# Optimization experiments

Hardware: AMD Instinct MI355X
Metric: run time of the kernel (lower is better)

## Reference

```python
import jax, jax.numpy as jnp
import numpy as np

B, S, HID = 8, 4096, 1024
NH, HD = 16, 64  # heads, head_dim
LN_EPS = 1e-12


def setup_inputs() -> dict:
    key = jax.random.key(0)
    ks = jax.random.split(key, 12)
    sd = 1.0 / np.sqrt(HID)
    return {
        "input_tensor": jax.random.normal(ks[0], (B, S, HID), jnp.float32),
        "attention_mask": jnp.ones((B, S), jnp.int32),
        "ln_gamma": jnp.ones((HID,), jnp.float32),
        "ln_beta": jnp.zeros((HID,), jnp.float32),
        "Wq": jax.random.normal(ks[1], (HID, HID), jnp.float32) * sd,
        "bq": jnp.zeros((HID,), jnp.float32),
        "Wk": jax.random.normal(ks[2], (HID, HID), jnp.float32) * sd,
        "bk": jnp.zeros((HID,), jnp.float32),
        "Wv": jax.random.normal(ks[3], (HID, HID), jnp.float32) * sd,
        "bv": jnp.zeros((HID,), jnp.float32),
        "Wo": jax.random.normal(ks[4], (HID, HID), jnp.float32) * sd,
        "bo": jnp.zeros((HID,), jnp.float32),
    }


def _layernorm(x, g, b):
    mu = jnp.mean(x, axis=-1, keepdims=True)
    var = jnp.mean(jnp.square(x - mu), axis=-1, keepdims=True)
    return (x - mu) * jax.lax.rsqrt(var + LN_EPS) * g + b


def reference(input_tensor, attention_mask, ln_gamma, ln_beta,
              Wq, bq, Wk, bk, Wv, bv, Wo, bo):
    # NOTE: attention_mask is accepted but unused, matching the original module.
    x = input_tensor
    x_norm = _layernorm(x, ln_gamma, ln_beta)
    # projections: query from normalized input, key/value from raw input
    q = (x_norm @ Wq.T + bq).reshape(B, S, NH, HD).transpose(0, 2, 1, 3)  # bhsd
    k = (x @ Wk.T + bk).reshape(B, S, NH, HD).transpose(0, 2, 1, 3)      # bhsd
    v = (x @ Wv.T + bv).reshape(B, S, NH, HD).transpose(0, 2, 1, 3)      # bhsd

    eq = jax.nn.elu(q)
    ek = jax.nn.elu(k)
    # per-token L2 norms over head_dim (matches norm over d in both layouts)
    eq = eq / jnp.linalg.norm(eq, axis=-1, keepdims=True)
    ek = ek / jnp.linalg.norm(ek, axis=-1, keepdims=True)

    # linear attention: Q (K^T V), never materializing [S,S]
    kv = jnp.einsum('bhsd,bhse->bhde', ek, v)          # [B,H,d,d]
    ctx = jnp.einsum('bhsd,bhde->bhse', eq, kv) / np.sqrt(HD)

    ctx = ctx.transpose(0, 2, 1, 3).reshape(B, S, HID)
    out = ctx @ Wo.T + bo
    return out + x  # residual (dropouts are identity in eval mode)
```

## Files before the change

### kernel.cpp

```cpp
#include <hip/hip_runtime.h>

typedef unsigned short u16;
typedef unsigned int   u32;
typedef __attribute__((ext_vector_type(8))) __bf16 bf16x8;
typedef __attribute__((ext_vector_type(4))) float  f32x4;

#define BQ   8
#define SQ   4096
#define NHQ  16
#define HIDD 1024
#define TOKN 32768

__device__ __forceinline__ u16 f2bf(float f){
  u32 u = __builtin_bit_cast(u32, f);
  u += 0x7fffu + ((u >> 16) & 1u);
  return (u16)(u >> 16);
}
__device__ __forceinline__ float bf2f(u16 h){
  return __builtin_bit_cast(float, (u32)h << 16);
}
__device__ __forceinline__ void gl16(const void* g, void* l){
  __builtin_amdgcn_global_load_lds((const __attribute__((address_space(1))) void*)g,
                                   (__attribute__((address_space(3))) void*)l, 16, 0, 0);
}
#define MFMA(a,b,c) __builtin_amdgcn_mfma_f32_16x16x32_bf16((a),(b),(c),0,0,0)

__global__ __launch_bounds__(256) void k_cast3(const float* __restrict__ wk,
    const float* __restrict__ wv, const float* __restrict__ wo,
    u16* __restrict__ okv, u16* __restrict__ oo){
  const int sel = blockIdx.x >> 10;
  const int i = ((blockIdx.x & 1023) << 8) + threadIdx.x;
  const float* in = (sel == 0) ? wk : (sel == 1) ? wv : wo;
  u16* o = (sel == 0) ? okv : (sel == 1) ? (okv + 1024 * 1024) : oo;
  float4 v = ((const float4*)in)[i];
  ushort4 r;
  r.x = f2bf(v.x); r.y = f2bf(v.y); r.z = f2bf(v.z); r.w = f2bf(v.w);
  ((ushort4*)o)[i] = r;
}

__global__ __launch_bounds__(256) void k_wq(const float* __restrict__ Wq,
    const float* __restrict__ gam, const float* __restrict__ bet, const float* __restrict__ bq,
    u16* __restrict__ wqb, float* __restrict__ cq, float* __restrict__ dq){
  const int j = blockIdx.x, t = threadIdx.x;
  const float4 wv = ((const float4*)(Wq + (size_t)j * 1024))[t];
  const float4 gv = ((const float4*)gam)[t];
  const float4 bv = ((const float4*)bet)[t];
  ushort4 r;
  r.x = f2bf(wv.x * gv.x); r.y = f2bf(wv.y * gv.y);
  r.z = f2bf(wv.z * gv.z); r.w = f2bf(wv.w * gv.w);
  ((ushort4*)(wqb + (size_t)j * 1024))[t] = r;
  float sc = bf2f(r.x) + bf2f(r.y) + bf2f(r.z) + bf2f(r.w);
  float sd = wv.x * bv.x + wv.y * bv.y + wv.z * bv.z + wv.w * bv.w;
  #pragma unroll
  for (int o = 1; o < 64; o <<= 1){ sc += __shfl_xor(sc, o); sd += __shfl_xor(sd, o); }
  __shared__ float sm[8];
  const int lane = t & 63, wid = t >> 6;
  if (lane == 0){ sm[wid] = sc; sm[wid + 4] = sd; }
  __syncthreads();
  if (t == 0){
    cq[j] = sm[0] + sm[1] + sm[2] + sm[3];
    dq[j] = sm[4] + sm[5] + sm[6] + sm[7] + bq[j];
  }
}

__global__ __launch_bounds__(256) void k_ln(const float* __restrict__ x,
    u16* __restrict__ xbf, float* __restrict__ mur, float* __restrict__ rsd){
  const int row = blockIdx.x, t = threadIdx.x;
  const float4 v = ((const float4*)(x + (size_t)row * HIDD))[t];
  float s  = v.x + v.y + v.z + v.w;
  float ss = v.x*v.x + v.y*v.y + v.z*v.z + v.w*v.w;
  #pragma unroll
  for (int o = 1; o < 64; o <<= 1){ s += __shfl_xor(s, o); ss += __shfl_xor(ss, o); }
  __shared__ float sm[8];
  const int lane = t & 63, wid = t >> 6;
  if (lane == 0){ sm[wid] = s; sm[wid + 4] = ss; }
  __syncthreads();
  s  = sm[0] + sm[1] + sm[2] + sm[3];
  ss = sm[4] + sm[5] + sm[6] + sm[7];
  const float mu   = s * (1.f / 1024.f);
  const float var  = ss * (1.f / 1024.f) - mu * mu;
  const float rstd = rsqrtf(var + 1e-12f);
  if (t == 0){ mur[row] = mu * rstd; rsd[row] = rstd; }
  ushort4 xo;
  xo.x = f2bf(v.x); xo.y = f2bf(v.y); xo.z = f2bf(v.z); xo.w = f2bf(v.w);
  ((ushort4*)(xbf + (size_t)row * HIDD))[t] = xo;
}

struct GP {
  const u16* A; const u16* W; const float* b1; const float* b2;
  int nsplit, lgNB, LDC, nblk; u16* outb; u16* voutT;
  const float* cq; const float* dq; const float* mur; const float* rsd;
};

template<int RES, int SPLIT>
__global__ __launch_bounds__(512, 2) void k_gemm256(GP p0, GP p1, int seg0,
    const u16* __restrict__ residb, float* __restrict__ outf){
  __shared__ union {
    u16 st[2][2][16384];
    float cep[8][1056];
    float cep2[8][2112];
  } sm;

  const GP& p = (blockIdx.x < seg0) ? p0 : p1;
  const int bseg = (blockIdx.x < seg0) ? blockIdx.x : blockIdx.x - seg0;
  const u16* __restrict__ A = p.A;
  const u16* __restrict__ W = p.W;
  const int lgNB = p.lgNB, LDC = p.LDC;

  const int wg = ((bseg & 7) * (p.nblk >> 3)) + (bseg >> 3);
  const int m0 = (wg >> lgNB) << 8;
  const int n0 = (wg & ((1 << lgNB) - 1)) << 8;

  const int t = threadIdx.x, lane = t & 63, wid = t >> 6;
  const int ln15 = lane & 15, hi = lane >> 4;
  const int wr = wid >> 2, wc = wid & 3;
  const int lg = lane & 7, lr = lane >> 3;

  auto stage = [&](int buf, int op, const u16* __restrict__ src, int rowoff, int kt){
    #pragma unroll
    for (int i = 0; i < 4; i++){
      const int cb  = ((i << 3) + wid) << 6;
      const int row = (cb >> 3) + lr;
      const int g   = lg ^ lr;
      gl16(src + (size_t)(rowoff + row) * HIDD + (kt << 6) + (g << 3),
           &sm.st[buf][op][cb << 3]);
    }
  };
  auto stageH = [&](int buf, int op, const u16* __restrict__ src, int rowoff, int kt, int half){
    #pragma unroll
    for (int i2 = 0; i2 < 2; i2++){
      const int i = (half << 1) + i2;
      const int cb  = ((i << 3) + wid) << 6;
      const int row = (cb >> 3) + lr;
      const int g   = lg ^ lr;
      gl16(src + (size_t)(rowoff + row) * HIDD + (kt << 6) + (g << 3),
           &sm.st[buf][op][cb << 3]);
    }
  };
  #define RD_A(c,m,ks) (*(const bf16x8*)&sm.st[c][0][(((wr << 7) + ((m) << 4) + ln15) << 6) + \
      (((((ks) << 2) + hi) ^ (lane & 7)) << 3)])
  #define RD_B(c,n,ks) (*(const bf16x8*)&sm.st[c][1][(((wc << 6) + ((n) << 4) + ln15) << 6) + \
      (((((ks) << 2) + hi) ^ (lane & 7)) << 3)])
  #define BARF do { asm volatile("" ::: "memory"); __builtin_amdgcn_s_barrier(); asm volatile("" ::: "memory"); } while(0)

  f32x4 acc[8][4] = {};

  stage(0, 0, A, m0, 0);
  stage(0, 1, W, n0, 0);
  stage(1, 1, W, n0, 1);
  asm volatile("s_waitcnt vmcnt(4)" ::: "memory");
  BARF;

  const int NT = HIDD / 64;
  if constexpr (SPLIT == 0){
    for (int kt = 0; kt < NT; ++kt){
      const int c = kt & 1;
      bf16x8 af[4][2], bq[4][2];
      #pragma unroll
      for (int m = 0; m < 4; m++){ af[m][0] = RD_A(c, m, 0); af[m][1] = RD_A(c, m, 1); }
      #pragma unroll
      for (int n = 0; n < 4; n++){ bq[n][0] = RD_B(c, n, 0); bq[n][1] = RD_B(c, n, 1); }
      const int ka = kt + 1 < NT ? kt + 1 : NT - 1;
      stage(c ^ 1, 0, A, m0, ka);
      __builtin_amdgcn_s_setprio(1);
      #pragma unroll
      for (int m = 0; m < 4; m++)
        #pragma unroll
        for (int n = 0; n < 4; n++){
          acc[m][n] = MFMA(af[m][0], bq[n][0], acc[m][n]);
          acc[m][n] = MFMA(af[m][1], bq[n][1], acc[m][n]);
        }
      __builtin_amdgcn_s_setprio(0);
      BARF;
      #pragma unroll
      for (int m = 0; m < 4; m++){ af[m][0] = RD_A(c, m + 4, 0); af[m][1] = RD_A(c, m + 4, 1); }
      const int kb = kt + 2 < NT ? kt + 2 : NT - 1;
      stage(c, 1, W, n0, kb);
      __builtin_amdgcn_s_setprio(1);
      #pragma unroll
      for (int m = 0; m < 4; m++)
        #pragma unroll
        for (int n = 0; n < 4; n++){
          acc[m + 4][n] = MFMA(af[m][0], bq[n][0], acc[m + 4][n]);
          acc[m + 4][n] = MFMA(af[m][1], bq[n][1], acc[m + 4][n]);
        }
      __builtin_amdgcn_s_setprio(0);
      asm volatile("s_waitcnt vmcnt(4)" ::: "memory");
      BARF;
    }
  } else {
    for (int kt = 0; kt < NT; ++kt){
      const int c = kt & 1;
      const int ka  = kt + 1 < NT ? kt + 1 : NT - 1;
      const int kb2 = kt + 2 < NT ? kt + 2 : NT - 1;
      bf16x8 af[2][2], bq[4][2];
      af[0][0] = RD_A(c, 0, 0); af[0][1] = RD_A(c, 0, 1);
      af[1][0] = RD_A(c, 1, 0); af[1][1] = RD_A(c, 1, 1);
      #pragma unroll
      for (int n = 0; n < 4; n++){ bq[n][0] = RD_B(c, n, 0); bq[n][1] = RD_B(c, n, 1); }
      stageH(c ^ 1, 0, A, m0, ka, 0);
      __builtin_amdgcn_s_setprio(1);
      #pragma unroll
      for (int m = 0; m < 2; m++)
        #pragma unroll
        for (int n = 0; n < 4; n++){
          acc[m][n] = MFMA(af[m][0], bq[n][0], acc[m][n]);
          acc[m][n] = MFMA(af[m][1], bq[n][1], acc[m][n]);
        }
      __builtin_amdgcn_s_setprio(0);
      BARF;
      af[0][0] = RD_A(c, 2, 0); af[0][1] = RD_A(c, 2, 1);
      af[1][0] = RD_A(c, 3, 0); af[1][1] = RD_A(c, 3, 1);
      stageH(c ^ 1, 0, A, m0, ka, 1);
      __builtin_amdgcn_s_setprio(1);
      #pragma unroll
      for (int m = 0; m < 2; m++)
        #pragma unroll
        for (int n = 0; n < 4; n++){
          acc[m + 2][n] = MFMA(af[m][0], bq[n][0], acc[m + 2][n]);
          acc[m + 2][n] = MFMA(af[m][1], bq[n][1], acc[m + 2][n]);
        }
      __builtin_amdgcn_s_setprio(0);
      BARF;
      af[0][0] = RD_A(c, 4, 0); af[0][1] = RD_A(c, 4, 1);
      af[1][0] = RD_A(c, 5, 0); af[1][1] = RD_A(c, 5, 1);
      stageH(c, 1, W, n0, kb2, 0);
      __builtin_amdgcn_s_setprio(1);
      #pragma unroll
      for (int m = 0; m < 2; m++)
        #pragma unroll
        for (int n = 0; n < 4; n++){
          acc[m + 4][n] = MFMA(af[m][0], bq[n][0], acc[m + 4][n]);
          acc[m + 4][n] = MFMA(af[m][1], bq[n][1], acc[m + 4][n]);
        }
      __builtin_amdgcn_s_setprio(0);
      BARF;
      af[0][0] = RD_A(c, 6, 0); af[0][1] = RD_A(c, 6, 1);
      af[1][0] = RD_A(c, 7, 0); af[1][1] = RD_A(c, 7, 1);
      stageH(c, 1, W, n0, kb2, 1);
      __builtin_amdgcn_s_setprio(1);
      #pragma unroll
      for (int m = 0; m < 2; m++)
        #pragma unroll
        for (int n = 0; n < 4; n++){
          acc[m + 6][n] = MFMA(af[m][0], bq[n][0], acc[m + 6][n]);
          acc[m + 6][n] = MFMA(af[m][1], bq[n][1], acc[m + 6][n]);
        }
      __builtin_amdgcn_s_setprio(0);
      asm volatile("s_waitcnt vmcnt(4)" ::: "memory");
      BARF;
    }
  }
  #undef RD_A
  #undef RD_B

  asm volatile("s_waitcnt vmcnt(0)" ::: "memory");
  BARF;

  const float* bp = (n0 < p.nsplit) ? p.b1 : (p.b2 - p.nsplit);
  float bn[4];
  #pragma unroll
  for (int n = 0; n < 4; n++) bn[n] = bp[n0 + (wc << 6) + (n << 4) + ln15];

  if constexpr (RES){
    float* cw = &sm.cep[wid][0];
    const int rr = lane >> 3, cb8 = (lane & 7) << 3;
    #pragma unroll
    for (int m = 0; m < 8; m++){
      #pragma unroll
      for (int n = 0; n < 4; n++)
        #pragma unroll
        for (int r = 0; r < 4; r++)
          cw[((hi << 2) + r) * 66 + (n << 4) + ln15] = acc[m][n][r] + bn[n];
      #pragma unroll
      for (int j = 0; j < 2; j++){
        const int row = (j << 3) + rr;
        const size_t gr = (size_t)(m0 + (wr << 7) + (m << 4) + row);
        const size_t gidx = gr * LDC + n0 + (wc << 6) + cb8;
        const size_t ridx = gr * HIDD + n0 + (wc << 6) + cb8;
        const uint4 rv = *(const uint4*)&residb[ridx];
        const u32 rr4[4] = {rv.x, rv.y, rv.z, rv.w};
        float4 o0, o1;
        o0.x = cw[row * 66 + cb8 + 0] + bf2f((u16)(rr4[0] & 0xffff));
        o0.y = cw[row * 66 + cb8 + 1] + bf2f((u16)(rr4[0] >> 16));
        o0.z = cw[row * 66 + cb8 + 2] + bf2f((u16)(rr4[1] & 0xffff));
        o0.w = cw[row * 66 + cb8 + 3] + bf2f((u16)(rr4[1] >> 16));
        o1.x = cw[row * 66 + cb8 + 4] + bf2f((u16)(rr4[2] & 0xffff));
        o1.y = cw[row * 66 + cb8 + 5] + bf2f((u16)(rr4[2] >> 16));
        o1.z = cw[row * 66 + cb8 + 6] + bf2f((u16)(rr4[3] & 0xffff));
        o1.w = cw[row * 66 + cb8 + 7] + bf2f((u16)(rr4[3] >> 16));
        *(float4*)&outf[gidx]     = o0;
        *(float4*)&outf[gidx + 4] = o1;
      }
    }
  } else if (p.voutT != nullptr && n0 >= p.nsplit){
    float* cw = &sm.cep2[wid][0];
    const int e0 = n0 - p.nsplit + (wc << 6);
    const int hh = e0 >> 6;
    u16* vt = p.voutT;
    #pragma unroll
    for (int mp = 0; mp < 4; mp++){
      #pragma unroll
      for (int mh = 0; mh < 2; mh++){
        const int m = (mp << 1) + mh;
        #pragma unroll
        for (int n = 0; n < 4; n++)
          #pragma unroll
          for (int r = 0; r < 4; r++)
            cw[((mh << 4) + (hi << 2) + r) * 66 + (n << 4) + ln15] = acc[m][n][r] + bn[n];
      }
      const int rg0 = m0 + (wr << 7) + (mp << 5);
      const int bb = rg0 >> 12, s0 = rg0 & 4095;
      u16* dst = vt + (((size_t)(bb << 4) + hh) * 64 + lane) * SQ + s0;
      #pragma unroll
      for (int j = 0; j < 4; j++){
        u32 ro[4];
        #pragma unroll
        for (int q = 0; q < 4; q++){
          float v0 = cw[((j << 3) + 2 * q    ) * 66 + lane];
          float v1 = cw[((j << 3) + 2 * q + 1) * 66 + lane];
          ro[q] = (u32)f2bf(v0) | ((u32)f2bf(v1) << 16);
        }
        uint4 o; o.x = ro[0]; o.y = ro[1]; o.z = ro[2]; o.w = ro[3];
        *(uint4*)&dst[j << 3] = o;
      }
    }
  } else {
    float* cw = &sm.cep[wid][0];
    const int rr = lane >> 3, cb8 = (lane & 7) << 3;
    u16* outb = p.outb;
    if (p.cq != nullptr){
      float cqn[4], dqn[4];
      #pragma unroll
      for (int n = 0; n < 4; n++){
        const int col = n0 + (wc << 6) + (n << 4) + ln15;
        cqn[n] = p.cq[col]; dqn[n] = p.dq[col];
      }
      #pragma unroll
      for (int m = 0; m < 8; m++){
        #pragma unroll
        for (int r = 0; r < 4; r++){
          const int grow = m0 + (wr << 7) + (m << 4) + (hi << 2) + r;
          const float mu = p.mur[grow], rs = p.rsd[grow];
          #pragma unroll
          for (int n = 0; n < 4; n++)
            cw[((hi << 2) + r) * 66 + (n << 4) + ln15] = rs * acc[m][n][r] - mu * cqn[n] + dqn[n];
        }
        #pragma unroll
        for (int j = 0; j < 2; j++){
          const int row = (j << 3) + rr;
          u32 ro[4];
          #pragma unroll
          for (int pq = 0; pq < 4; pq++){
            float v0 = cw[row * 66 + cb8 + 2 * pq];
            float v1 = cw[row * 66 + cb8 + 2 * pq + 1];
            ro[pq] = (u32)f2bf(v0) | ((u32)f2bf(v1) << 16);
          }
          uint4 o; o.x = ro[0]; o.y = ro[1]; o.z = ro[2]; o.w = ro[3];
          *(uint4*)&outb[(size_t)(m0 + (wr << 7) + (m << 4) + row) * LDC
                         + n0 + (wc << 6) + cb8] = o;
        }
      }
    } else {
      #pragma unroll
      for (int m = 0; m < 8; m++){
        #pragma unroll
        for (int n = 0; n < 4; n++)
          #pragma unroll
          for (int r = 0; r < 4; r++)
            cw[((hi << 2) + r) * 66 + (n << 4) + ln15] = acc[m][n][r] + bn[n];
        #pragma unroll
        for (int j = 0; j < 2; j++){
          const int row = (j << 3) + rr;
          u32 ro[4];
          #pragma unroll
          for (int pq = 0; pq < 4; pq++){
            float v0 = cw[row * 66 + cb8 + 2 * pq];
            float v1 = cw[row * 66 + cb8 + 2 * pq + 1];
            ro[pq] = (u32)f2bf(v0) | ((u32)f2bf(v1) << 16);
          }
          uint4 o; o.x = ro[0]; o.y = ro[1]; o.z = ro[2]; o.w = ro[3];
          *(uint4*)&outb[(size_t)(m0 + (wr << 7) + (m << 4) + row) * LDC
                         + n0 + (wc << 6) + cb8] = o;
        }
      }
    }
  }
  #undef BARF
}

__global__ __launch_bounds__(256) void k_transposeK(const u16* __restrict__ kb,
                                                    u16* __restrict__ ekT){
  __shared__ float tile[64][65];
  __shared__ float pr[64][4];
  __shared__ float rn[64];
  const int sb = blockIdx.x << 6, h = blockIdx.y, b = blockIdx.z;
  const int t = threadIdx.x;
  {
    const int tok = t >> 2, q = t & 3;
    const u16* src = kb + (size_t)(b * SQ + sb + tok) * 1024 + (h << 6) + (q << 4);
    uint4 u0 = *(const uint4*)src;
    uint4 u1 = *(const uint4*)(src + 8);
    u32 uu[8] = {u0.x, u0.y, u0.z, u0.w, u1.x, u1.y, u1.z, u1.w};
    float ss = 0.f;
    #pragma unroll
    for (int i = 0; i < 8; i++){
      float f0 = bf2f((u16)(uu[i] & 0xffff));
      float f1 = bf2f((u16)(uu[i] >> 16));
      f0 = f0 > 0.f ? f0 : expm1f(f0);
      f1 = f1 > 0.f ? f1 : expm1f(f1);
      ss += f0 * f0 + f1 * f1;
      tile[tok][(q << 4) + 2*i]     = f0;
      tile[tok][(q << 4) + 2*i + 1] = f1;
    }
    pr[tok][q] = ss;
  }
  __syncthreads();
  if (t < 64) rn[t] = rsqrtf(pr[t][0] + pr[t][1] + pr[t][2] + pr[t][3]);
  __syncthreads();
  const int d = t >> 2, sq2 = (t & 3) << 4;
  u16* dst = ekT + ((size_t)(b * NHQ + h) * 64 + d) * SQ + sb + sq2;
  u32 ro[8];
  #pragma unroll
  for (int i = 0; i < 8; i++){
    float v0 = tile[sq2 + 2*i][d]     * rn[sq2 + 2*i];
    float v1 = tile[sq2 + 2*i + 1][d] * rn[sq2 + 2*i + 1];
    ro[i] = (u32)f2bf(v0) | ((u32)f2bf(v1) << 16);
  }
  uint4 o0; o0.x = ro[0]; o0.y = ro[1]; o0.z = ro[2]; o0.w = ro[3];
  uint4 o1; o1.x = ro[4]; o1.y = ro[5]; o1.z = ro[6]; o1.w = ro[7];
  *(uint4*)dst = o0;
  *(uint4*)(dst + 8) = o1;
}

__global__ __launch_bounds__(256) void k_kv(const u16* __restrict__ vT, const u16* __restrict__ ekT,
                                            u16* __restrict__ kvT){
  const int bh = blockIdx.x;
  const u16* Av = vT  + (size_t)bh * 64 * SQ;
  const u16* Bk = ekT + (size_t)bh * 64 * SQ;
  const int lane = threadIdx.x & 63, wid = threadIdx.x >> 6;
  const int ln15 = lane & 15, hi = lane >> 4;
  f32x4 acc[4][4] = {};
  const int kb = wid << 10;
  for (int ks = 0; ks < 32; ++ks){
    const int k0 = kb + (ks << 5) + (hi << 3);
    bf16x8 af[4], bfr[4];
    #pragma unroll
    for (int m = 0; m < 4; m++) af[m]  = *(const bf16x8*)(Av + (size_t)((m << 4) + ln15) * SQ + k0);
    #pragma unroll
    for (int n = 0; n < 4; n++) bfr[n] = *(const bf16x8*)(Bk + (size_t)((n << 4) + ln15) * SQ + k0);
    #pragma unroll
    for (int m = 0; m < 4; m++)
      #pragma unroll
      for (int n = 0; n < 4; n++)
        acc[m][n] = MFMA(af[m], bfr[n], acc[m][n]);
  }
  __shared__ float red[64][64];
  for (int w = 0; w < 4; ++w){
    if (wid == w){
      #pragma unroll
      for (int m = 0; m < 4; m++)
        #pragma unroll
        for (int n = 0; n < 4; n++)
          #pragma unroll
          for (int r = 0; r < 4; r++){
            int row = (m << 4) + (hi << 2) + r;
            int col = (n << 4) + ln15;
            if (w == 0) red[row][col] = acc[m][n][r];
            else        red[row][col] += acc[m][n][r];
          }
    }
    __syncthreads();
  }
  u16* dst = kvT + (size_t)bh * 4096;
  const int tt = threadIdx.x;
  #pragma unroll
  for (int i = 0; i < 16; i++){
    int idx = tt * 16 + i;
    dst[idx] = f2bf(red[idx >> 6][idx & 63] * 0.125f);
  }
}

__global__ __launch_bounds__(256) void k_ctx(const u16* __restrict__ q, const u16* __restrict__ kvT,
                                             u16* __restrict__ ctx){
  __shared__ u16 Alds[1024 * 8];
  __shared__ u16 Blds[512 * 8];
  __shared__ float prn[128][2];
  const int sb = blockIdx.x << 7;
  const int h = blockIdx.y, b = blockIdx.z;
  const int bh = (b << 4) + h;
  const int t = threadIdx.x, lane = t & 63, wid = t >> 6;
  const int ln15 = lane & 15, hi = lane >> 4;
  {
    uint4 va[4]; uint4 vb[2];
    #pragma unroll
    for (int i = 0; i < 4; i++){
      int c = (wid << 6) + (i << 8) + lane;
      int g = c >> 7, row = c & 127;
      va[i] = *(const uint4*)(q + (size_t)(b * SQ + sb + row) * HIDD + (h << 6) + g * 8);
    }
    #pragma unroll
    for (int i = 0; i < 2; i++){
      int c = (wid << 6) + (i << 8) + lane;
      int g = c >> 6, row = c & 63;
      vb[i] = *(const uint4*)(kvT + (size_t)bh * 4096 + (row << 6) + g * 8);
    }
    #pragma unroll
    for (int i = 0; i < 4; i++)
      *(uint4*)&Alds[((wid << 6) + (i << 8) + lane) * 8] = va[i];
    #pragma unroll
    for (int i = 0; i < 2; i++)
      *(uint4*)&Blds[((wid << 6) + (i << 8) + lane) * 8] = vb[i];
  }
  __syncthreads();
  {
    const int row = t & 127, half = t >> 7;
    float vals[4][8]; float ss = 0.f;
    #pragma unroll
    for (int g4 = 0; g4 < 4; g4++){
      const int g = (half << 2) + g4;
      uint4 u = *(const uint4*)&Alds[((g << 7) + row) * 8];
      u32 uu[4] = {u.x, u.y, u.z, u.w};
      #pragma unroll
      for (int i = 0; i < 4; i++){
        float f0 = bf2f((u16)(uu[i] & 0xffff));
        float f1 = bf2f((u16)(uu[i] >> 16));
        f0 = f0 > 0.f ? f0 : expm1f(f0);
        f1 = f1 > 0.f ? f1 : expm1f(f1);
        vals[g4][2*i] = f0; vals[g4][2*i+1] = f1;
        ss += f0 * f0 + f1 * f1;
      }
    }
    prn[row][half] = ss;
    __syncthreads();
    const float rn = rsqrtf(prn[row][0] + prn[row][1]);
    #pragma unroll
    for (int g4 = 0; g4 < 4; g4++){
      const int g = (half << 2) + g4;
      u32 ro[4];
      #pragma unroll
      for (int i = 0; i < 4; i++)
        ro[i] = (u32)f2bf(vals[g4][2*i] * rn) | ((u32)f2bf(vals[g4][2*i+1] * rn) << 16);
      uint4 o; o.x = ro[0]; o.y = ro[1]; o.z = ro[2]; o.w = ro[3];
      *(uint4*)&Alds[((g << 7) + row) * 8] = o;
    }
  }
  __syncthreads();
  f32x4 acc[2][4] = {};
  #pragma unroll
  for (int k2 = 0; k2 < 2; k2++){
    const int g = (k2 << 2) + hi;
    bf16x8 af[2], bfr[4];
    #pragma unroll
    for (int m = 0; m < 2; m++) af[m]  = *(const bf16x8*)&Alds[((g << 7) + (wid << 5) + (m << 4) + ln15) * 8];
    #pragma unroll
    for (int n = 0; n < 4; n++) bfr[n] = *(const bf16x8*)&Blds[((g << 6) + (n << 4) + ln15) * 8];
    #pragma unroll
    for (int m = 0; m < 2; m++)
      #pragma unroll
      for (int n = 0; n < 4; n++)
        acc[m][n] = MFMA(af[m], bfr[n], acc[m][n]);
  }
  #pragma unroll
  for (int m = 0; m < 2; m++)
    #pragma unroll
    for (int n = 0; n < 4; n++)
      #pragma unroll
      for (int r = 0; r < 4; r++){
        int srow = sb + (wid << 5) + (m << 4) + (hi << 2) + r;
        int col  = (n << 4) + ln15;
        ctx[(size_t)(b * SQ + srow) * HIDD + (h << 6) + col] = f2bf(acc[m][n][r]);
      }
}

extern "C" void kernel_launch(void* const* d_in, const int* in_sizes, int n_in,
                              void* d_out, int out_size, void* d_ws, size_t ws_size,
                              hipStream_t stream){
  const float* x   = (const float*)d_in[0];
  const float* lng = (const float*)d_in[2];
  const float* lnb = (const float*)d_in[3];
  const float* Wq  = (const float*)d_in[4];
  const float* bq  = (const float*)d_in[5];
  const float* Wk  = (const float*)d_in[6];
  const float* bk  = (const float*)d_in[7];
  const float* Wv  = (const float*)d_in[8];
  const float* bv  = (const float*)d_in[9];
  const float* Wo  = (const float*)d_in[10];
  const float* bo  = (const float*)d_in[11];
  float* out = (float*)d_out;

  char* w = (char*)d_ws;
  const size_t MB = 1ull << 20;
  u16* wqb  = (u16*)(w + 0   * MB);
  u16* wkvb = (u16*)(w + 2   * MB);
  u16* wob  = (u16*)(w + 6   * MB);
  u16* xbf  = (u16*)(w + 8   * MB);
  u16* xnbf = (u16*)(w + 72  * MB);
  u16* qb   = (u16*)(w + 136 * MB);
  u16* kb   = (u16*)(w + 200 * MB);
  u16* vT   = (u16*)(w + 264 * MB);
  u16* kvT  = (u16*)(w + 328 * MB);
  float* murstd = (float*)(w + 330 * MB);
  float* rstdv  = (float*)(w + 331 * MB);
  float* cqv    = (float*)(w + 332 * MB);
  float* dqv    = (float*)(w + 333 * MB);
  u16* ekT = xnbf;
  u16* ctx = kb;

  k_cast3<<<3072, 256, 0, stream>>>(Wk, Wv, Wo, wkvb, wob);
  k_wq<<<1024, 256, 0, stream>>>(Wq, lng, lnb, bq, wqb, cqv, dqv);
  k_ln<<<TOKN, 256, 0, stream>>>(x, xbf, murstd, rstdv);

  GP pq  = { xbf, wqb,  bq, bq, 1 << 30, 2, 1024, 512,  qb, nullptr, cqv, dqv, murstd, rstdv };
  GP pkv = { xbf, wkvb, bk, bv, 1024,    3, 1024, 1024, kb, vT,      nullptr, nullptr, nullptr, nullptr };
  k_gemm256<0, 0><<<1536, 512, 0, stream>>>(pq, pkv, 512, nullptr, nullptr);

  k_transposeK<<<dim3(64, 16, 8), 256, 0, stream>>>(kb, ekT);
  k_kv<<<128, 256, 0, stream>>>(vT, ekT, kvT);
  k_ctx<<<dim3(32, 16, 8), 256, 0, stream>>>(qb, kvT, ctx);

  GP po = { ctx, wob, bo, bo, 1 << 30, 2, 1024, 512, nullptr, nullptr,
            nullptr, nullptr, nullptr, nullptr };
  k_gemm256<1, 1><<<512, 512, 0, stream>>>(po, po, 512, xbf, out);

  (void)in_sizes; (void)n_in; (void)out_size; (void)ws_size;
}
```

Baseline: 675.7 us.

## Fuse ELU, L2-normalize and transpose of K into the KV reduction kernel

Removes the separate k_transposeK kernel and its 64 MB ekT intermediate. k_kv now reads K tokens directly, applies ELU and per-token L2 normalization using shuffle reductions, and transposes through a per-wave LDS tile before the MFMA. This saves one launch and a full write and read of transposed K. The trade-off is that k_kv runs only 128 blocks, so it now does the extra ELU/expm1 work and strided global loads on low occupancy, which may make that kernel the bottleneck.

```diff
diff --git a/kernel.cpp b/kernel.cpp
--- a/kernel.cpp
+++ b/kernel.cpp
@@ -389,73 +389,54 @@
   #undef BARF
 }
 
-__global__ __launch_bounds__(256) void k_transposeK(const u16* __restrict__ kb,
-                                                    u16* __restrict__ ekT){
-  __shared__ float tile[64][65];
-  __shared__ float pr[64][4];
-  __shared__ float rn[64];
-  const int sb = blockIdx.x << 6, h = blockIdx.y, b = blockIdx.z;
-  const int t = threadIdx.x;
-  {
-    const int tok = t >> 2, q = t & 3;
-    const u16* src = kb + (size_t)(b * SQ + sb + tok) * 1024 + (h << 6) + (q << 4);
-    uint4 u0 = *(const uint4*)src;
-    uint4 u1 = *(const uint4*)(src + 8);
-    u32 uu[8] = {u0.x, u0.y, u0.z, u0.w, u1.x, u1.y, u1.z, u1.w};
-    float ss = 0.f;
-    #pragma unroll
-    for (int i = 0; i < 8; i++){
-      float f0 = bf2f((u16)(uu[i] & 0xffff));
-      float f1 = bf2f((u16)(uu[i] >> 16));
-      f0 = f0 > 0.f ? f0 : expm1f(f0);
-      f1 = f1 > 0.f ? f1 : expm1f(f1);
-      ss += f0 * f0 + f1 * f1;
-      tile[tok][(q << 4) + 2*i]     = f0;
-      tile[tok][(q << 4) + 2*i + 1] = f1;
-    }
-    pr[tok][q] = ss;
-  }
-  __syncthreads();
-  if (t < 64) rn[t] = rsqrtf(pr[t][0] + pr[t][1] + pr[t][2] + pr[t][3]);
-  __syncthreads();
-  const int d = t >> 2, sq2 = (t & 3) << 4;
-  u16* dst = ekT + ((size_t)(b * NHQ + h) * 64 + d) * SQ + sb + sq2;
-  u32 ro[8];
-  #pragma unroll
-  for (int i = 0; i < 8; i++){
-    float v0 = tile[sq2 + 2*i][d]     * rn[sq2 + 2*i];
-    float v1 = tile[sq2 + 2*i + 1][d] * rn[sq2 + 2*i + 1];
-    ro[i] = (u32)f2bf(v0) | ((u32)f2bf(v1) << 16);
-  }
-  uint4 o0; o0.x = ro[0]; o0.y = ro[1]; o0.z = ro[2]; o0.w = ro[3];
-  uint4 o1; o1.x = ro[4]; o1.y = ro[5]; o1.z = ro[6]; o1.w = ro[7];
-  *(uint4*)dst = o0;
-  *(uint4*)(dst + 8) = o1;
-}
-
-__global__ __launch_bounds__(256) void k_kv(const u16* __restrict__ vT, const u16* __restrict__ ekT,
+__global__ __launch_bounds__(256) void k_kv(const u16* __restrict__ vT, const u16* __restrict__ kb,
                                             u16* __restrict__ kvT){
-  const int bh = blockIdx.x;
-  const u16* Av = vT  + (size_t)bh * 64 * SQ;
-  const u16* Bk = ekT + (size_t)bh * 64 * SQ;
+  __shared__ u16 trans[4][64][40];
+  __shared__ float red[64][64];
+  const int bh = blockIdx.x, b = bh >> 4, h = bh & 15;
+  const u16* Av = vT + (size_t)bh * 64 * SQ;
   const int lane = threadIdx.x & 63, wid = threadIdx.x >> 6;
   const int ln15 = lane & 15, hi = lane >> 4;
+  const int dg = lane & 7, sr = lane >> 3;
   f32x4 acc[4][4] = {};
-  const int kb = wid << 10;
-  for (int ks = 0; ks < 32; ++ks){
-    const int k0 = kb + (ks << 5) + (hi << 3);
+  const int sbase = wid << 10;
+  for (int ts = 0; ts < 32; ++ts){
+    const int s0 = sbase + (ts << 5);
+    #pragma unroll
+    for (int pass = 0; pass < 4; ++pass){
+      const int sl = (pass << 3) + sr;
+      const uint4 u = *(const uint4*)(kb + (size_t)(b * SQ + s0 + sl) * 1024
+                                      + (h << 6) + (dg << 3));
+      u32 uu[4] = {u.x, u.y, u.z, u.w};
+      float e[8]; float ss = 0.f;
+      #pragma unroll
+      for (int i = 0; i < 4; i++){
+        float f0 = bf2f((u16)(uu[i] & 0xffff));
+        float f1 = bf2f((u16)(uu[i] >> 16));
+        f0 = f0 > 0.f ? f0 : expm1f(f0);
+        f1 = f1 > 0.f ? f1 : expm1f(f1);
+        e[2*i] = f0; e[2*i+1] = f1;
+        ss += f0 * f0 + f1 * f1;
+      }
+      ss += __shfl_xor(ss, 1); ss += __shfl_xor(ss, 2); ss += __shfl_xor(ss, 4);
+      const float rn = rsqrtf(ss);
+      #pragma unroll
+      for (int i = 0; i < 8; i++)
+        trans[wid][(dg << 3) + i][sl] = f2bf(e[i] * rn);
+    }
     bf16x8 af[4], bfr[4];
     #pragma unroll
-    for (int m = 0; m < 4; m++) af[m]  = *(const bf16x8*)(Av + (size_t)((m << 4) + ln15) * SQ + k0);
-    #pragma unroll
-    for (int n = 0; n < 4; n++) bfr[n] = *(const bf16x8*)(Bk + (size_t)((n << 4) + ln15) * SQ + k0);
+    for (int m = 0; m < 4; m++)
+      af[m] = *(const bf16x8*)(Av + (size_t)((m << 4) + ln15) * SQ + s0 + (hi << 3));
+    #pragma unroll
+    for (int n = 0; n < 4; n++)
+      bfr[n] = *(const bf16x8*)&trans[wid][(n << 4) + ln15][hi << 3];
     #pragma unroll
     for (int m = 0; m < 4; m++)
       #pragma unroll
       for (int n = 0; n < 4; n++)
         acc[m][n] = MFMA(af[m], bfr[n], acc[m][n]);
   }
-  __shared__ float red[64][64];
   for (int w = 0; w < 4; ++w){
     if (wid == w){
       #pragma unroll
@@ -595,7 +576,6 @@
   u16* wkvb = (u16*)(w + 2   * MB);
   u16* wob  = (u16*)(w + 6   * MB);
   u16* xbf  = (u16*)(w + 8   * MB);
-  u16* xnbf = (u16*)(w + 72  * MB);
   u16* qb   = (u16*)(w + 136 * MB);
   u16* kb   = (u16*)(w + 200 * MB);
   u16* vT   = (u16*)(w + 264 * MB);
@@ -604,7 +584,6 @@
   float* rstdv  = (float*)(w + 331 * MB);
   float* cqv    = (float*)(w + 332 * MB);
   float* dqv    = (float*)(w + 333 * MB);
-  u16* ekT = xnbf;
   u16* ctx = kb;
 
   k_cast3<<<3072, 256, 0, stream>>>(Wk, Wv, Wo, wkvb, wob);
@@ -615,8 +594,7 @@
   GP pkv = { xbf, wkvb, bk, bv, 1024,    3, 1024, 1024, kb, vT,      nullptr, nullptr, nullptr, nullptr };
   k_gemm256<0, 0><<<1536, 512, 0, stream>>>(pq, pkv, 512, nullptr, nullptr);
 
-  k_transposeK<<<dim3(64, 16, 8), 256, 0, stream>>>(kb, ekT);
-  k_kv<<<128, 256, 0, stream>>>(vT, ekT, kvT);
+  k_kv<<<128, 256, 0, stream>>>(vT, kb, kvT);
   k_ctx<<<dim3(32, 16, 8), 256, 0, stream>>>(qb, kvT, ctx);
 
   GP po = { ctx, wob, bo, bo, 1 << 30, 2, 1024, 512, nullptr, nullptr,
```

Result: slower. 737.2 us (+9.1%).
